# Performance work log

Measured on AMD Instinct MI355X. Metric: run time of the kernel, lower is better.

Reference implementation:

```python
import jax, jax.numpy as jnp
from jax import lax
import numpy as np

B, T, A = 8192, 512, 4  # sessions, trials, n_actions


def setup_inputs() -> dict:
    key = jax.random.key(0)
    k1, k2, k3 = jax.random.split(key, 3)
    choices = jax.random.randint(k1, (B, T), 0, A)
    actions = jax.nn.one_hot(choices, A, dtype=jnp.float32)          # one-hot actions
    rew = (jax.random.uniform(k2, (B, T)) < 0.5).astype(jnp.float32)  # binary rewards
    rewards = jnp.broadcast_to(rew[..., None], (B, T, A))
    inputs = jnp.concatenate([actions, rewards], axis=-1)            # [B,T,2A]
    params_raw = jax.random.normal(k3, (13,), jnp.float32) * 0.5
    return {"inputs": inputs, "params_raw": params_raw}


def _transform(p):
    sp, sg = jax.nn.softplus, jax.nn.sigmoid
    return dict(
        beta_r=jnp.clip(sp(p[0]), 0.01, 20.0),
        lapse=jnp.clip(sg(p[1]), 0.01, 0.99),
        prior=jnp.clip(sp(p[2]), 0.01, 0.99),
        alpha=jnp.clip(sg(p[3]), 0.01, 0.99),
        decay=jnp.clip(sg(p[4]), 0.01, 0.99),
        ab1=p[5], ab2=p[6],
        pers=sp(p[7]), sw=p[8],
        gamma=sp(p[10]),
        temp=jnp.clip(sp(p[11]) + 1e-6, 1e-6, 100.0),
        beta_p=sp(p[12]),
    )


def _forward(inputs, params_raw):
    pr = _transform(params_raw)
    nb = inputs.shape[0]
    actions_t = jnp.swapaxes(inputs[..., :A], 0, 1)   # [T,B,A]
    rewards_t = jnp.swapaxes(inputs[..., A:2 * A], 0, 1)

    q0 = jnp.ones((nb, A), jnp.float32) * pr["prior"]
    old0 = jnp.full((nb,), -1, jnp.int32)
    tsls0 = jnp.zeros((nb,), jnp.float32)
    expl0 = jnp.full((nb,), 1.0, jnp.float32) * pr["alpha"]
    cum0 = jnp.zeros((nb, A), jnp.float32)

    def step(carry, xr):
        q, old, tsls, expl, cum = carry
        a, r = xr
        cc = jnp.argmax(a, axis=-1).astype(jnp.int32)          # current choice
        oh = jax.nn.one_hot(cc, A, dtype=q.dtype)
        rv = jnp.sum(r * a, axis=-1)                            # reward value
        delta = rv - pr["gamma"] * (1.0 - rv) - jnp.sum(q * oh, axis=-1)
        q = q + delta[:, None] * oh                             # Q update (full overwrite of error)
        same = cc == old
        tsls = jnp.where(same, tsls + 1.0, 0.0)
        expl = expl * (1.0 - 1e-3)                              # exploration decay
        cum = cum + oh
        qm = jnp.mean(q, axis=-1, keepdims=True)
        q = (1.0 - expl[:, None]) * q + expl[:, None] * qm      # mean-mixing exploration
        q = q * pr["decay"]
        probs = (1.0 - pr["lapse"]) * jax.nn.softmax(
            pr["beta_r"] * q / pr["temp"] + pr["beta_p"] * jnp.log1p(cum), axis=-1
        ) + pr["lapse"] / A
        logits = jnp.log(probs)
        oh_old = jax.nn.one_hot(old, A, dtype=q.dtype)          # zeros when old == -1
        bonus = (
            (jnp.where(same, pr["pers"], pr["sw"]))[:, None] * oh
            + pr["ab1"] * oh_old
            + pr["ab2"] * jax.nn.one_hot((cc + 2) % A, A, dtype=q.dtype)
            + oh * jnp.log(tsls + 1.0)[:, None]
        )
        return (q, cc, tsls, expl, cum), logits + bonus

    _, logits_t = lax.scan(step, (q0, old0, tsls0, expl0, cum0), (actions_t, rewards_t))
    return jnp.swapaxes(logits_t, 0, 1)  # [B,T,A]


def reference(inputs, params_raw):
    return _forward(inputs, params_raw)
```

## Files before the change

kernel.cpp:

```cpp
#include <hip/hip_runtime.h>
#include <math.h>

constexpr int B_ = 8192;
constexpr int T_ = 512;
constexpr int CH = 16;
constexpr int NCH = T_ / CH;

__device__ __forceinline__ float sp_(float x) {
    return fmaxf(x, 0.0f) + log1pf(expf(-fabsf(x)));
}
__device__ __forceinline__ float sg_(float x) { return 1.0f / (1.0f + expf(-x)); }
__device__ __forceinline__ float clipf(float x, float lo, float hi) { return fminf(fmaxf(x, lo), hi); }
__device__ __forceinline__ float sel(bool c, float a, float b) { return c ? a : b; }

__global__ __launch_bounds__(256, 4) void castro_one(const float* __restrict__ in,
                                                     const float* __restrict__ p,
                                                     float* __restrict__ out) {
    __shared__ char smem[8 * 4 * 33 * 16];
    uint4* cc4 = reinterpret_cast<uint4*>(smem);
    uint4* rr4 = reinterpret_cast<uint4*>(smem) + 256;
    unsigned char* ccb = reinterpret_cast<unsigned char*>(cc4);
    unsigned char* rrb = reinterpret_cast<unsigned char*>(rr4);
    float4* stg = reinterpret_cast<float4*>(smem);

    const int tid = threadIdx.x;
    const int b0  = blockIdx.x * 8;

    const float4* __restrict__ in4 = reinterpret_cast<const float4*>(in) + (size_t)b0 * 1024;
#pragma unroll
    for (int it = 0; it < 32; ++it) {
        const int idx  = it * 256 + tid;
        const float4 fv = in4[idx];
        const int sess = idx >> 10;
        const int step = (idx & 1023) >> 1;
        if ((idx & 1) == 0) {
            ccb[sess * 512 + step] =
                (unsigned char)(fv.y > 0.5f ? 1 : (fv.z > 0.5f ? 2 : (fv.w > 0.5f ? 3 : 0)));
        } else {
            rrb[sess * 512 + step] = (fv.x > 0.5f) ? 4 : 0;
        }
    }
    __syncthreads();

    const int w    = tid >> 6;
    const int lane = tid & 63;
    const int k    = lane & 31;
    const int sess = w * 2 + (lane >> 5);
    const int b    = b0 + sess;

    const float beta_r = clipf(sp_(p[0]), 0.01f, 20.0f);
    const float lapse  = clipf(sg_(p[1]), 0.01f, 0.99f);
    const float prior  = clipf(sp_(p[2]), 0.01f, 0.99f);
    const float alpha  = clipf(sg_(p[3]), 0.01f, 0.99f);
    const float decay  = clipf(sg_(p[4]), 0.01f, 0.99f);
    const float ab1    = p[5];
    const float ab2    = p[6];
    const float pers   = sp_(p[7]);
    const float sw     = p[8];
    const float gamma  = sp_(p[10]);
    const float temp   = clipf(sp_(p[11]) + 1e-6f, 1e-6f, 100.0f);
    const float beta_p = sp_(p[12]);
    const float brt = beta_r / temp;
    const float l4  = lapse * 0.25f;
    const float oml = 1.0f - lapse;

    const float e0k = alpha * __powf(1.0f - 1e-3f, (float)(CH * k));

    uint4 cw;
    {
        const uint4 c4 = cc4[sess * 32 + k];
        const uint4 r4 = rr4[sess * 32 + k];
        cw.x = c4.x | r4.x; cw.y = c4.y | r4.y; cw.z = c4.z | r4.z; cw.w = c4.w | r4.w;
    }
    __syncthreads();

    float m[4][4], v[4], n[4];
#pragma unroll
    for (int i = 0; i < 4; ++i) {
#pragma unroll
        for (int j = 0; j < 4; ++j) m[i][j] = (i == j) ? 1.0f : 0.0f;
        v[i] = 0.0f; n[i] = 0.0f;
    }
    int prev = -1, run = 0;
    float e = e0k;

#pragma unroll
    for (int ti = 0; ti < CH; ++ti) {
        const unsigned word = (ti < 4) ? cw.x : (ti < 8) ? cw.y : (ti < 12) ? cw.z : cw.w;
        const unsigned byte = (word >> (8 * (ti & 3))) & 0xffu;
        const int  cc = (int)(byte & 3u);
        const bool rf = (byte & 4u) != 0u;
        const float tgt = rf ? 1.0f : -gamma;
        e *= (1.0f - 1e-3f);
        run = (cc == prev) ? (run + 1) : 1;
        prev = cc;
#pragma unroll
        for (int i = 0; i < 4; ++i) {
            const bool hit = (i == cc);
            v[i] = hit ? tgt : v[i];
            n[i] += hit ? 1.0f : 0.0f;
#pragma unroll
            for (int j = 0; j < 4; ++j) m[i][j] = hit ? 0.0f : m[i][j];
        }
        const float aa = decay * (1.0f - e);
        const float bf = decay * e * 0.25f;
        float csum[4];
#pragma unroll
        for (int j = 0; j < 4; ++j) csum[j] = bf * ((m[0][j] + m[1][j]) + (m[2][j] + m[3][j]));
        const float vs = bf * ((v[0] + v[1]) + (v[2] + v[3]));
#pragma unroll
        for (int i = 0; i < 4; ++i) {
#pragma unroll
            for (int j = 0; j < 4; ++j) m[i][j] = fmaf(aa, m[i][j], csum[j]);
            v[i] = fmaf(aa, v[i], vs);
        }
    }

    float sm[4][4], sv[4];
#pragma unroll
    for (int i = 0; i < 4; ++i) {
#pragma unroll
        for (int j = 0; j < 4; ++j) sm[i][j] = m[i][j];
        sv[i] = v[i];
    }
#pragma unroll
    for (int d = 1; d < 32; d <<= 1) {
        float pm[4][4], pv[4];
#pragma unroll
        for (int i = 0; i < 4; ++i) {
#pragma unroll
            for (int j = 0; j < 4; ++j) pm[i][j] = __shfl_up(sm[i][j], d, 32);
            pv[i] = __shfl_up(sv[i], d, 32);
        }
        if (k >= d) {
            float nm[4][4], nv[4];
#pragma unroll
            for (int i = 0; i < 4; ++i) {
#pragma unroll
                for (int j = 0; j < 4; ++j)
                    nm[i][j] = fmaf(sm[i][0], pm[0][j], fmaf(sm[i][1], pm[1][j],
                               fmaf(sm[i][2], pm[2][j], sm[i][3] * pm[3][j])));
                nv[i] = fmaf(sm[i][0], pv[0], fmaf(sm[i][1], pv[1],
                        fmaf(sm[i][2], pv[2], fmaf(sm[i][3], pv[3], sv[i]))));
            }
#pragma unroll
            for (int i = 0; i < 4; ++i) {
#pragma unroll
                for (int j = 0; j < 4; ++j) sm[i][j] = nm[i][j];
                sv[i] = nv[i];
            }
        }
    }

    float q[4];
#pragma unroll
    for (int i = 0; i < 4; ++i) {
        float er0 = __shfl_up(sm[i][0], 1, 32);
        float er1 = __shfl_up(sm[i][1], 1, 32);
        float er2 = __shfl_up(sm[i][2], 1, 32);
        float er3 = __shfl_up(sm[i][3], 1, 32);
        float ev  = __shfl_up(sv[i], 1, 32);
        if (k == 0) { er0 = (i == 0); er1 = (i == 1); er2 = (i == 2); er3 = (i == 3); ev = 0.0f; }
        q[i] = fmaf(prior, ((er0 + er1) + (er2 + er3)), ev);
    }

    float cex[4];
#pragma unroll
    for (int i = 0; i < 4; ++i) {
        float s = n[i];
#pragma unroll
        for (int d = 1; d < 32; d <<= 1) {
            const float t = __shfl_up(s, d, 32);
            if (k >= d) s += t;
        }
        cex[i] = s - n[i];
    }

    const float lcf  = (float)prev;
    const float runf = (float)run;
    float lcm1 = __shfl_up(lcf, 1, 32);
    if (k == 0) lcm1 = -1.0f;
    const bool u = (runf == 16.0f) && (lcf == lcm1);
    const unsigned long long bal = __ballot(u);
    const unsigned gm = (unsigned)(bal >> (lane & 32));
    const unsigned vsh = (k == 31) ? gm : (gm << (31 - k));
    const int c = __clz(~vsh);
    const float runsrc = __shfl(runf, (lane & 32) + (k - c));
    const float TR = 16.0f * (float)c + runsrc;
    float TRm1 = __shfl_up(TR, 1, 32);
    const float tslsS = (k == 0) ? 0.0f : (TRm1 - 1.0f);
    const float lcprev = (k == 0) ? -1.0f : lcm1;

    float q0 = q[0], q1 = q[1], q2 = q[2], q3 = q[3];
    float c0 = cex[0], c1 = cex[1], c2 = cex[2], c3 = cex[3];
    float tsls = tslsS;
    float expl = e0k;
    int oldc = (int)lcprev;

    float4* __restrict__ out4 = reinterpret_cast<float4*>(out);

#pragma unroll
    for (int h = 0; h < 4; ++h) {
#pragma unroll
        for (int tl = 0; tl < 4; ++tl) {
            const int ti = h * 4 + tl;
            const unsigned word = (ti < 4) ? cw.x : (ti < 8) ? cw.y : (ti < 12) ? cw.z : cw.w;
            const unsigned byte = (word >> (8 * (ti & 3))) & 0xffu;
            const int  cc = (int)(byte & 3u);
            const bool rf = (byte & 4u) != 0u;
            const float target = sel(rf, 1.0f, -gamma);
            const int prv = oldc;
            const bool same = (cc == oldc);
            tsls = sel(same, tsls + 1.0f, 0.0f);
            expl *= (1.0f - 1e-3f);
            const bool i0 = (cc == 0), i1 = (cc == 1), i2 = (cc == 2), i3 = (cc == 3);
            q0 = sel(i0, target, q0);  c0 += sel(i0, 1.0f, 0.0f);
            q1 = sel(i1, target, q1);  c1 += sel(i1, 1.0f, 0.0f);
            q2 = sel(i2, target, q2);  c2 += sel(i2, 1.0f, 0.0f);
            q3 = sel(i3, target, q3);  c3 += sel(i3, 1.0f, 0.0f);
            const float qm  = 0.25f * ((q0 + q1) + (q2 + q3));
            const float omd = (1.0f - expl) * decay;
            const float eqd = (expl * decay) * qm;
            q0 = fmaf(omd, q0, eqd);
            q1 = fmaf(omd, q1, eqd);
            q2 = fmaf(omd, q2, eqd);
            q3 = fmaf(omd, q3, eqd);
            oldc = cc;

            const float s0 = fmaf(brt, q0, beta_p * __logf(1.0f + c0));
            const float s1 = fmaf(brt, q1, beta_p * __logf(1.0f + c1));
            const float s2 = fmaf(brt, q2, beta_p * __logf(1.0f + c2));
            const float s3 = fmaf(brt, q3, beta_p * __logf(1.0f + c3));
            const float mx = fmaxf(fmaxf(s0, s1), fmaxf(s2, s3));
            const float e0 = __expf(s0 - mx);
            const float e1 = __expf(s1 - mx);
            const float e2 = __expf(s2 - mx);
            const float e3 = __expf(s3 - mx);
            const float iz = oml / ((e0 + e1) + (e2 + e3));

            float l0 = __logf(fmaf(e0, iz, l4));
            float l1 = __logf(fmaf(e1, iz, l4));
            float l2 = __logf(fmaf(e2, iz, l4));
            float l3 = __logf(fmaf(e3, iz, l4));

            const float bcc = sel(same, pers, sw) + __logf(tsls + 1.0f);
            const int cc2 = cc ^ 2;
            l0 += sel(i0, bcc, 0.0f) + sel(prv == 0, ab1, 0.0f) + sel(cc2 == 0, ab2, 0.0f);
            l1 += sel(i1, bcc, 0.0f) + sel(prv == 1, ab1, 0.0f) + sel(cc2 == 1, ab2, 0.0f);
            l2 += sel(i2, bcc, 0.0f) + sel(prv == 2, ab1, 0.0f) + sel(cc2 == 2, ab2, 0.0f);
            l3 += sel(i3, bcc, 0.0f) + sel(prv == 3, ab1, 0.0f) + sel(cc2 == 3, ab2, 0.0f);

            stg[(sess * 4 + tl) * 33 + k] = make_float4(l0, l1, l2, l3);
        }

        __syncthreads();
#pragma unroll
        for (int j = 0; j < 4; ++j) {
            const int s  = tid >> 5;
            const int ee = j * 32 + (tid & 31);
            const int kk = ee >> 2;
            const int tl = ee & 3;
            const float4 val = stg[(s * 4 + tl) * 33 + kk];
            out4[(size_t)(b0 + s) * T_ + kk * CH + h * 4 + tl] = val;
        }
        __syncthreads();
    }
}

extern "C" void kernel_launch(void* const* d_in, const int* in_sizes, int n_in,
                              void* d_out, int out_size, void* d_ws, size_t ws_size,
                              hipStream_t stream) {
    const float* inputs = (const float*)d_in[0];
    const float* params = (const float*)d_in[1];
    float* out = (float*)d_out;

    castro_one<<<dim3(B_ / 8), dim3(256), 0, stream>>>(inputs, params, out);
}
```

Before: 73.49 us.

## Map one session per 64-lane wave with 8-step chunks

Halves the per-lane chunk length from 16 to 8 trials and gives each session a full 64-lane wavefront instead of half a wave. Blocks now cover 4 sessions, so the grid doubles. The serial recurrence per lane gets shorter and more threads are in flight, which should hide memory and latency better. In exchange the 4x4 affine-matrix prefix scan gains a sixth shuffle level, and the ballot and run-length logic moves to 64-bit masks.

New measurement: 71.92 us. 2.1% less time.

```diff
diff --git a/kernel.cpp b/kernel.cpp
--- a/kernel.cpp
+++ b/kernel.cpp
@@ -3,7 +3,7 @@
 
 constexpr int B_ = 8192;
 constexpr int T_ = 512;
-constexpr int CH = 16;
+constexpr int CH = 8;
 constexpr int NCH = T_ / CH;
 
 __device__ __forceinline__ float sp_(float x) {
@@ -16,19 +16,19 @@
 __global__ __launch_bounds__(256, 4) void castro_one(const float* __restrict__ in,
                                                      const float* __restrict__ p,
                                                      float* __restrict__ out) {
-    __shared__ char smem[8 * 4 * 33 * 16];
-    uint4* cc4 = reinterpret_cast<uint4*>(smem);
-    uint4* rr4 = reinterpret_cast<uint4*>(smem) + 256;
-    unsigned char* ccb = reinterpret_cast<unsigned char*>(cc4);
-    unsigned char* rrb = reinterpret_cast<unsigned char*>(rr4);
+    __shared__ char smem[4 * 4 * 65 * 16];
+    uint2* cc2 = reinterpret_cast<uint2*>(smem);
+    uint2* rr2 = reinterpret_cast<uint2*>(smem) + 256;
+    unsigned char* ccb = reinterpret_cast<unsigned char*>(cc2);
+    unsigned char* rrb = reinterpret_cast<unsigned char*>(rr2);
     float4* stg = reinterpret_cast<float4*>(smem);
 
     const int tid = threadIdx.x;
-    const int b0  = blockIdx.x * 8;
+    const int b0  = blockIdx.x * 4;
 
     const float4* __restrict__ in4 = reinterpret_cast<const float4*>(in) + (size_t)b0 * 1024;
 #pragma unroll
-    for (int it = 0; it < 32; ++it) {
+    for (int it = 0; it < 16; ++it) {
         const int idx  = it * 256 + tid;
         const float4 fv = in4[idx];
         const int sess = idx >> 10;
@@ -42,10 +42,8 @@
     }
     __syncthreads();
 
-    const int w    = tid >> 6;
-    const int lane = tid & 63;
-    const int k    = lane & 31;
-    const int sess = w * 2 + (lane >> 5);
+    const int sess = tid >> 6;
+    const int k    = tid & 63;
     const int b    = b0 + sess;
 
     const float beta_r = clipf(sp_(p[0]), 0.01f, 20.0f);
@@ -66,11 +64,11 @@
 
     const float e0k = alpha * __powf(1.0f - 1e-3f, (float)(CH * k));
 
-    uint4 cw;
+    uint2 cw;
     {
-        const uint4 c4 = cc4[sess * 32 + k];
-        const uint4 r4 = rr4[sess * 32 + k];
-        cw.x = c4.x | r4.x; cw.y = c4.y | r4.y; cw.z = c4.z | r4.z; cw.w = c4.w | r4.w;
+        const uint2 c2 = cc2[sess * 64 + k];
+        const uint2 r2 = rr2[sess * 64 + k];
+        cw.x = c2.x | r2.x; cw.y = c2.y | r2.y;
     }
     __syncthreads();
 
@@ -86,7 +84,7 @@
 
 #pragma unroll
     for (int ti = 0; ti < CH; ++ti) {
-        const unsigned word = (ti < 4) ? cw.x : (ti < 8) ? cw.y : (ti < 12) ? cw.z : cw.w;
+        const unsigned word = (ti < 4) ? cw.x : cw.y;
         const unsigned byte = (word >> (8 * (ti & 3))) & 0xffu;
         const int  cc = (int)(byte & 3u);
         const bool rf = (byte & 4u) != 0u;
@@ -124,13 +122,13 @@
         sv[i] = v[i];
     }
 #pragma unroll
-    for (int d = 1; d < 32; d <<= 1) {
+    for (int d = 1; d < 64; d <<= 1) {
         float pm[4][4], pv[4];
 #pragma unroll
         for (int i = 0; i < 4; ++i) {
 #pragma unroll
-            for (int j = 0; j < 4; ++j) pm[i][j] = __shfl_up(sm[i][j], d, 32);
-            pv[i] = __shfl_up(sv[i], d, 32);
+            for (int j = 0; j < 4; ++j) pm[i][j] = __shfl_up(sm[i][j], d, 64);
+            pv[i] = __shfl_up(sv[i], d, 64);
         }
         if (k >= d) {
             float nm[4][4], nv[4];
@@ -155,11 +153,11 @@
     float q[4];
 #pragma unroll
     for (int i = 0; i < 4; ++i) {
-        float er0 = __shfl_up(sm[i][0], 1, 32);
-        float er1 = __shfl_up(sm[i][1], 1, 32);
-        float er2 = __shfl_up(sm[i][2], 1, 32);
-        float er3 = __shfl_up(sm[i][3], 1, 32);
-        float ev  = __shfl_up(sv[i], 1, 32);
+        float er0 = __shfl_up(sm[i][0], 1, 64);
+        float er1 = __shfl_up(sm[i][1], 1, 64);
+        float er2 = __shfl_up(sm[i][2], 1, 64);
+        float er3 = __shfl_up(sm[i][3], 1, 64);
+        float ev  = __shfl_up(sv[i], 1, 64);
         if (k == 0) { er0 = (i == 0); er1 = (i == 1); er2 = (i == 2); er3 = (i == 3); ev = 0.0f; }
         q[i] = fmaf(prior, ((er0 + er1) + (er2 + er3)), ev);
     }
@@ -169,8 +167,8 @@
     for (int i = 0; i < 4; ++i) {
         float s = n[i];
 #pragma unroll
-        for (int d = 1; d < 32; d <<= 1) {
-            const float t = __shfl_up(s, d, 32);
+        for (int d = 1; d < 64; d <<= 1) {
+            const float t = __shfl_up(s, d, 64);
             if (k >= d) s += t;
         }
         cex[i] = s - n[i];
@@ -178,16 +176,15 @@
 
     const float lcf  = (float)prev;
     const float runf = (float)run;
-    float lcm1 = __shfl_up(lcf, 1, 32);
+    float lcm1 = __shfl_up(lcf, 1, 64);
     if (k == 0) lcm1 = -1.0f;
-    const bool u = (runf == 16.0f) && (lcf == lcm1);
+    const bool u = (runf == 8.0f) && (lcf == lcm1);
     const unsigned long long bal = __ballot(u);
-    const unsigned gm = (unsigned)(bal >> (lane & 32));
-    const unsigned vsh = (k == 31) ? gm : (gm << (31 - k));
-    const int c = __clz(~vsh);
-    const float runsrc = __shfl(runf, (lane & 32) + (k - c));
-    const float TR = 16.0f * (float)c + runsrc;
-    float TRm1 = __shfl_up(TR, 1, 32);
+    const unsigned long long vsh = (k == 63) ? bal : (bal << (63 - k));
+    const int c = __clzll(~vsh);
+    const float runsrc = __shfl(runf, k - c, 64);
+    const float TR = 8.0f * (float)c + runsrc;
+    float TRm1 = __shfl_up(TR, 1, 64);
     const float tslsS = (k == 0) ? 0.0f : (TRm1 - 1.0f);
     const float lcprev = (k == 0) ? -1.0f : lcm1;
 
@@ -200,11 +197,11 @@
     float4* __restrict__ out4 = reinterpret_cast<float4*>(out);
 
 #pragma unroll
-    for (int h = 0; h < 4; ++h) {
+    for (int h = 0; h < 2; ++h) {
 #pragma unroll
         for (int tl = 0; tl < 4; ++tl) {
             const int ti = h * 4 + tl;
-            const unsigned word = (ti < 4) ? cw.x : (ti < 8) ? cw.y : (ti < 12) ? cw.z : cw.w;
+            const unsigned word = (ti < 4) ? cw.x : cw.y;
             const unsigned byte = (word >> (8 * (ti & 3))) & 0xffu;
             const int  cc = (int)(byte & 3u);
             const bool rf = (byte & 4u) != 0u;
@@ -250,17 +247,17 @@
             l2 += sel(i2, bcc, 0.0f) + sel(prv == 2, ab1, 0.0f) + sel(cc2 == 2, ab2, 0.0f);
             l3 += sel(i3, bcc, 0.0f) + sel(prv == 3, ab1, 0.0f) + sel(cc2 == 3, ab2, 0.0f);
 
-            stg[(sess * 4 + tl) * 33 + k] = make_float4(l0, l1, l2, l3);
+            stg[(sess * 4 + tl) * 65 + k] = make_float4(l0, l1, l2, l3);
         }
 
         __syncthreads();
 #pragma unroll
         for (int j = 0; j < 4; ++j) {
-            const int s  = tid >> 5;
-            const int ee = j * 32 + (tid & 31);
-            const int kk = ee >> 2;
-            const int tl = ee & 3;
-            const float4 val = stg[(s * 4 + tl) * 33 + kk];
+            const int s   = tid >> 6;
+            const int ee  = j * 64 + (tid & 63);
+            const int kk  = ee >> 2;
+            const int tl  = ee & 3;
+            const float4 val = stg[(s * 4 + tl) * 65 + kk];
             out4[(size_t)(b0 + s) * T_ + kk * CH + h * 4 + tl] = val;
         }
         __syncthreads();
@@ -274,5 +271,5 @@
     const float* params = (const float*)d_in[1];
     float* out = (float*)d_out;
 
-    castro_one<<<dim3(B_ / 8), dim3(256), 0, stream>>>(inputs, params, out);
+    castro_one<<<dim3(B_ / 4), dim3(256), 0, stream>>>(inputs, params, out);
 }
```
